# Kernel optimization log

Hardware: AMD Instinct MI355X
Metric: run time of the kernel (lower is better)

The kernel has to match this reference:

```python
import jax, jax.numpy as jnp
import numpy as np

N_NODES = 50000
N_EDGES = 800000
IN_CH = 128
HID = 32
HEADS = 4
LATENT = 64
NEG_SLOPE = 0.2  # PyG GATConv default


def setup_inputs() -> dict:
    key = jax.random.key(0)
    ks = jax.random.split(key, 12)
    HC = HID * HEADS
    inp = {
        "x": jax.random.normal(ks[0], (N_NODES, IN_CH), dtype=jnp.float32),
        "edge_index": jax.random.randint(ks[1], (2, N_EDGES), 0, N_NODES, dtype=jnp.int64),
        # GATConv params
        "W_gat": jax.random.normal(ks[2], (IN_CH, HC), dtype=jnp.float32) / np.sqrt(IN_CH),
        "b_gat": jnp.zeros((HC,), dtype=jnp.float32),
        "att_src": jax.random.normal(ks[3], (HEADS, HID), dtype=jnp.float32) / np.sqrt(HID),
        "att_dst": jax.random.normal(ks[4], (HEADS, HID), dtype=jnp.float32) / np.sqrt(HID),
        # encoder / decoder / output linears
        "W_enc": jax.random.normal(ks[5], (HC, LATENT), dtype=jnp.float32) / np.sqrt(HC),
        "b_enc": jnp.zeros((LATENT,), dtype=jnp.float32),
        "W_dec": jax.random.normal(ks[6], (LATENT, HC), dtype=jnp.float32) / np.sqrt(LATENT),
        "b_dec": jnp.zeros((HC,), dtype=jnp.float32),
        "W_out": jax.random.normal(ks[7], (HC, IN_CH), dtype=jnp.float32) / np.sqrt(HC),
        "b_out": jnp.zeros((IN_CH,), dtype=jnp.float32),
    }
    return inp


def reference(x, edge_index, W_gat, b_gat, att_src, att_dst,
              W_enc, b_enc, W_dec, b_dec, W_out, b_out):
    N = x.shape[0]
    H, C = att_src.shape
    # PyG GATConv adds self-loops by default
    loops = jnp.arange(N, dtype=edge_index.dtype)
    src = jnp.concatenate([edge_index[0], loops])  # message sources (x_j)
    dst = jnp.concatenate([edge_index[1], loops])  # aggregation targets (x_i)

    h = (x @ W_gat).reshape(N, H, C)               # [N,H,C]
    a_src = jnp.einsum('nhc,hc->nh', h, att_src)   # [N,H]
    a_dst = jnp.einsum('nhc,hc->nh', h, att_dst)   # [N,H]

    e = jax.nn.leaky_relu(a_src[src] + a_dst[dst], NEG_SLOPE)  # [E,H]
    # segment softmax over destination nodes (numerically stable)
    e_max = jax.ops.segment_max(e, dst, num_segments=N)
    e_exp = jnp.exp(e - e_max[dst])
    denom = jax.ops.segment_sum(e_exp, dst, num_segments=N)
    alpha = e_exp / (denom[dst] + 1e-16)           # [E,H]

    msg = h[src] * alpha[:, :, None]               # [E,H,C]
    agg = jax.ops.segment_sum(msg, dst, num_segments=N)  # [N,H,C]
    gat_out = agg.reshape(N, H * C) + b_gat        # concat heads + bias

    x1 = jax.nn.elu(gat_out)
    encoded = x1 @ W_enc + b_enc
    decoded = encoded @ W_dec + b_dec
    x2 = jax.nn.elu(decoded)
    return x2 @ W_out + b_out
```

## Files before the change

### kernel.cpp

```cpp
#include <hip/hip_runtime.h>
#include <hip/hip_bf16.h>

#define N_NODES 50000
#define N_EDGES 800000
#define BM 64
#define NBUCK 196
#define CAP 6144
#define CHUNK 2048
#define NB_BUCKET_BLOCKS ((N_EDGES + CHUNK - 1) / CHUNK)
#define SWZ_BLOCKS 192
#define SWZ_G 32768
#define BFT 1024

typedef _Float16 half4v __attribute__((ext_vector_type(4)));
typedef _Float16 half8 __attribute__((ext_vector_type(8)));
typedef float    float4v __attribute__((ext_vector_type(4)));

__device__ __forceinline__ float elu_f(float v) {
    return (v > 0.f) ? v : (__expf(v) - 1.f);
}

__device__ __forceinline__ unsigned f2bf2(float a, float b) {
    unsigned ua = __float_as_uint(a), ub = __float_as_uint(b);
    ua = (ua + 0x7FFFu + ((ua >> 16) & 1u)) >> 16;
    ub = (ub + 0x7FFFu + ((ub >> 16) & 1u)) >> 16;
    return ua | (ub << 16);
}
__device__ __forceinline__ float2 bf2f2(unsigned u) {
    float2 f;
    f.x = __uint_as_float(u << 16);
    f.y = __uint_as_float(u & 0xFFFF0000u);
    return f;
}

__global__ __launch_bounds__(256) void k_pre(const void* __restrict__ e_raw,
        int* __restrict__ flag,
        const float* __restrict__ We, const float* __restrict__ Wd,
        const float* __restrict__ Wo, const float* __restrict__ Wg,
        _Float16* __restrict__ swz, int* __restrict__ bcursor) {
    const int b = blockIdx.x;
    const int tid = threadIdx.x;
    if (b >= SWZ_BLOCKS) {
        __shared__ int nz;
        if (tid == 0) nz = 0;
        bcursor[tid] = 0;
        __syncthreads();
        int cnt = 0;
        const unsigned* er = (const unsigned*)e_raw;
        for (int i = tid; i < 2048; i += 256)
            if (er[2 * i + 1] != 0u) cnt = 1;
        if (cnt) atomicOr(&nz, 1);
        __syncthreads();
        if (tid == 0) *flag = (nz == 0) ? 1 : 0;
        return;
    }
    int t = b * 256 + tid;
    const float* W; int base, N;
    if (t < 8192)       { W = We; base = 0;     N = 64;  }
    else if (t < 16384) { W = Wd; base = 8192;  N = 128; }
    else if (t < 32768) { W = Wo; base = 16384; N = 128; }
    else                { W = Wg; base = SWZ_G; N = 128; }
    int loc = t - base;
    int nnt = N >> 4;
    int frag = loc >> 9, r = loc & 511, lane = r >> 3, j = r & 7;
    int kc = frag / nnt, nt = frag - kc * nnt;
    int k = kc * 32 + ((lane >> 4) << 3) + j;
    int n = nt * 16 + (lane & 15);
    swz[t] = (_Float16)W[k * N + n];
}

__global__ __launch_bounds__(256) void k_gat_lin(const float* __restrict__ x,
        const _Float16* __restrict__ swz, const float* __restrict__ att_s,
        const float* __restrict__ att_d, unsigned* __restrict__ h_bf,
        float* __restrict__ a_src, float* __restrict__ a_dst) {
    __shared__ _Float16 sx[64 * 128];
    __shared__ float sh[64 * 132];
    const int tid = threadIdx.x;
    const int m0 = blockIdx.x * 64;

#pragma unroll
    for (int i = 0; i < 8; i++) {
        int idx = tid + i * 256;
        int r = idx >> 5, c4 = idx & 31;
        int row = m0 + r; if (row >= N_NODES) row = N_NODES - 1;
        float4 v = ((const float4*)(x + (size_t)row * 128))[c4];
        half4v h;
        h[0] = (_Float16)v.x; h[1] = (_Float16)v.y;
        h[2] = (_Float16)v.z; h[3] = (_Float16)v.w;
        *(half4v*)&sx[r * 128 + c4 * 4] = h;
    }
    __syncthreads();

    const int wave = tid >> 6, lane = tid & 63;
    const int lm = lane & 15, lq = lane >> 4;
    const int wrow = wave * 16;

    {
        float4v acc[8];
#pragma unroll
        for (int nt = 0; nt < 8; nt++) acc[nt] = (float4v){0.f, 0.f, 0.f, 0.f};
#pragma unroll
        for (int kc = 0; kc < 4; kc++) {
            half8 a = *(const half8*)&sx[(wrow + lm) * 128 + kc * 32 + lq * 8];
#pragma unroll
            for (int nt = 0; nt < 8; nt++) {
                half8 b = *(const half8*)&swz[SWZ_G + (kc * 8 + nt) * 512 + lane * 8];
                acc[nt] = __builtin_amdgcn_mfma_f32_16x16x32_f16(a, b, acc[nt], 0, 0, 0);
            }
        }
#pragma unroll
        for (int nt = 0; nt < 8; nt++)
#pragma unroll
            for (int r = 0; r < 4; r++)
                sh[(wrow + lq * 4 + r) * 132 + nt * 16 + lm] = acc[nt][r];
    }
    __syncthreads();

    const int c0 = (tid & 31) * 4;
    const int r0 = (tid >> 5) * 8;
    float4 as4 = *(const float4*)&att_s[c0];
    float4 ad4 = *(const float4*)&att_d[c0];
    const int head = c0 >> 5;

#pragma unroll
    for (int r = 0; r < 8; r++) {
        int row = m0 + r0 + r;
        bool ok = row < N_NODES;
        float4 hv = *(const float4*)&sh[(r0 + r) * 132 + c0];
        if (ok) {
            uint2 p;
            p.x = f2bf2(hv.x, hv.y);
            p.y = f2bf2(hv.z, hv.w);
            *(uint2*)&h_bf[(size_t)row * 64 + (c0 >> 1)] = p;
        }
        float vs = hv.x * as4.x + hv.y * as4.y + hv.z * as4.z + hv.w * as4.w;
        float vd = hv.x * ad4.x + hv.y * ad4.y + hv.z * ad4.z + hv.w * ad4.w;
#pragma unroll
        for (int o = 4; o >= 1; o >>= 1) {
            vs += __shfl_down(vs, o, 8);
            vd += __shfl_down(vd, o, 8);
        }
        if (ok && (tid & 7) == 0) {
            a_src[row * 4 + head] = vs;
            a_dst[row * 4 + head] = vd;
        }
    }
}

__global__ __launch_bounds__(256) void k_bucket(const void* __restrict__ e_raw,
        const int* __restrict__ flag, int* __restrict__ bcursor,
        uint2* __restrict__ ebuck) {
    __shared__ int lh[256];
    __shared__ int gbase[256];
    __shared__ int lcur[256];
    const int tid = threadIdx.x;
    const int base = blockIdx.x * CHUNK;
    const int is64 = *flag;
    const long long* e64 = (const long long*)e_raw;
    const int* e32 = (const int*)e_raw;

    lh[tid] = 0;
    __syncthreads();
#pragma unroll 4
    for (int j = 0; j < CHUNK / 256; j++) {
        int e = base + j * 256 + tid;
        if (e < N_EDGES) {
            int d = is64 ? (int)e64[N_EDGES + e] : e32[N_EDGES + e];
            atomicAdd(&lh[d >> 8], 1);
        }
    }
    __syncthreads();
    if (lh[tid]) gbase[tid] = atomicAdd(&bcursor[tid], lh[tid]);
    lcur[tid] = 0;
    __syncthreads();
#pragma unroll 4
    for (int j = 0; j < CHUNK / 256; j++) {
        int e = base + j * 256 + tid;
        if (e < N_EDGES) {
            int sN, d;
            if (is64) { sN = (int)e64[e]; d = (int)e64[N_EDGES + e]; }
            else      { sN = e32[e];      d = e32[N_EDGES + e]; }
            int b = d >> 8;
            int idx = gbase[b] + atomicAdd(&lcur[b], 1);
            if (idx < CAP) {
                uint2 pr; pr.x = (unsigned)sN; pr.y = (unsigned)d;
                ebuck[b * CAP + idx] = pr;
            }
        }
    }
}

__global__ __launch_bounds__(BFT) void k_bfill(const uint2* __restrict__ ebuck,
        const int* __restrict__ bcursor, int2* __restrict__ nodeoff,
        int* __restrict__ csr_src) {
    __shared__ int lh[256];
    __shared__ int lexc[256];
    __shared__ int lcur[256];
    const int tid = threadIdx.x;
    const int b = blockIdx.x;
    const int lo = b * CAP;
    int cnt = bcursor[b]; if (cnt > CAP) cnt = CAP;
    const int hi = lo + cnt;
    const int n0 = b << 8;

    if (tid < 256) { lh[tid] = 0; lcur[tid] = 0; }
    __syncthreads();
    for (int i = lo + tid; i < hi; i += BFT)
        atomicAdd(&lh[ebuck[i].y & 255], 1);
    __syncthreads();
    {
        int v = 0;
        if (tid < 256) { v = lh[tid]; lexc[tid] = v; }
        __syncthreads();
        for (int o = 1; o < 256; o <<= 1) {
            int u = (tid < 256 && tid >= o) ? lexc[tid - o] : 0;
            __syncthreads();
            if (tid < 256) lexc[tid] += u;
            __syncthreads();
        }
        if (tid < 256) {
            int s = lexc[tid] - v;
            lexc[tid] = s;
            int node = n0 + tid;
            if (node < N_NODES) {
                int2 no; no.x = lo + s; no.y = v;
                nodeoff[node] = no;
            }
        }
    }
    __syncthreads();
    for (int i = lo + tid; i < hi; i += BFT) {
        uint2 pr = ebuck[i];
        int li = (int)(pr.y & 255);
        int p = atomicAdd(&lcur[li], 1);
        csr_src[lo + lexc[li] + p] = (int)pr.x;
    }
}

__global__ __launch_bounds__(256) void k_gather(const int2* __restrict__ nodeoff,
        const int* __restrict__ csr_src, const float* __restrict__ a_src,
        const float* __restrict__ a_dst, const unsigned* __restrict__ h_bf,
        float* __restrict__ agg) {
    int d = blockIdx.x * 4 + (threadIdx.x >> 6);
    if (d >= N_NODES) return;
    const int lane = threadIdx.x & 63;
    const int half = lane >> 5;
    const int l32 = lane & 31;
    const int hd = l32 >> 3;
    int2 nd = nodeoff[d];
    const int lo = nd.x, hi = nd.x + nd.y;

    const float adh = a_dst[d * 4 + hd];

    float den = 0.f;
    float ax = 0.f, ay = 0.f, az = 0.f, aw = 0.f;

    if (half == 0) {
        float t = a_src[d * 4 + hd] + adh;
        t = t > 0.f ? t : 0.2f * t;
        float es = __expf(t);
        den = es;
        uint2 hu = ((const uint2*)(h_bf + (size_t)d * 64))[l32];
        float2 c01 = bf2f2(hu.x), c23 = bf2f2(hu.y);
        ax = c01.x * es; ay = c01.y * es;
        az = c23.x * es; aw = c23.y * es;
    }

    int base = lo;
    for (; base + 8 <= hi; base += 8) {
        int i0 = base + half;
        int s0 = csr_src[i0 + 0];
        int s1 = csr_src[i0 + 2];
        int s2 = csr_src[i0 + 4];
        int s3 = csr_src[i0 + 6];
        uint2 u0 = ((const uint2*)(h_bf + (size_t)s0 * 64))[l32];
        uint2 u1 = ((const uint2*)(h_bf + (size_t)s1 * 64))[l32];
        uint2 u2 = ((const uint2*)(h_bf + (size_t)s2 * 64))[l32];
        uint2 u3 = ((const uint2*)(h_bf + (size_t)s3 * 64))[l32];
        float a0 = a_src[s0 * 4 + hd];
        float a1 = a_src[s1 * 4 + hd];
        float a2 = a_src[s2 * 4 + hd];
        float a3 = a_src[s3 * 4 + hd];

        float t0 = a0 + adh; t0 = t0 > 0.f ? t0 : 0.2f * t0;
        float t1 = a1 + adh; t1 = t1 > 0.f ? t1 : 0.2f * t1;
        float t2 = a2 + adh; t2 = t2 > 0.f ? t2 : 0.2f * t2;
        float t3 = a3 + adh; t3 = t3 > 0.f ? t3 : 0.2f * t3;
        float e0 = __expf(t0);
        float e1 = __expf(t1);
        float e2 = __expf(t2);
        float e3 = __expf(t3);
        den += (e0 + e1) + (e2 + e3);

        float2 p, q;
        p = bf2f2(u0.x); q = bf2f2(u0.y);
        ax = fmaf(p.x, e0, ax); ay = fmaf(p.y, e0, ay);
        az = fmaf(q.x, e0, az); aw = fmaf(q.y, e0, aw);
        p = bf2f2(u1.x); q = bf2f2(u1.y);
        ax = fmaf(p.x, e1, ax); ay = fmaf(p.y, e1, ay);
        az = fmaf(q.x, e1, az); aw = fmaf(q.y, e1, aw);
        p = bf2f2(u2.x); q = bf2f2(u2.y);
        ax = fmaf(p.x, e2, ax); ay = fmaf(p.y, e2, ay);
        az = fmaf(q.x, e2, az); aw = fmaf(q.y, e2, aw);
        p = bf2f2(u3.x); q = bf2f2(u3.y);
        ax = fmaf(p.x, e3, ax); ay = fmaf(p.y, e3, ay);
        az = fmaf(q.x, e3, az); aw = fmaf(q.y, e3, aw);
    }
    for (int i = base + half; i < hi; i += 2) {
        int s = csr_src[i];
        float tt = a_src[s * 4 + hd] + adh;
        tt = tt > 0.f ? tt : 0.2f * tt;
        float e = __expf(tt);
        den += e;
        uint2 hu = ((const uint2*)(h_bf + (size_t)s * 64))[l32];
        float2 p = bf2f2(hu.x), q = bf2f2(hu.y);
        ax = fmaf(p.x, e, ax); ay = fmaf(p.y, e, ay);
        az = fmaf(q.x, e, az); aw = fmaf(q.y, e, aw);
    }

    den += __shfl_xor(den, 32);
    ax += __shfl_xor(ax, 32);
    ay += __shfl_xor(ay, 32);
    az += __shfl_xor(az, 32);
    aw += __shfl_xor(aw, 32);

    if (half == 0) {
        float inv = 1.f / (den + 1e-16f);
        float4 o; o.x = ax * inv; o.y = ay * inv; o.z = az * inv; o.w = aw * inv;
        ((float4*)(agg + (size_t)d * 128))[l32] = o;
    }
}

__global__ __launch_bounds__(256) void k_mlp(const float* __restrict__ agg,
        const float* __restrict__ b_gat, const _Float16* __restrict__ swz,
        const float* __restrict__ b_enc, const float* __restrict__ b_dec,
        const float* __restrict__ b_out, float* __restrict__ out) {
    __shared__ _Float16 sx[64 * 128];
    __shared__ _Float16 se[4 * 16 * 64];
    const int tid = threadIdx.x;
    const int m0 = blockIdx.x * 64;

#pragma unroll
    for (int i = 0; i < 8; i++) {
        int idx = tid + i * 256;
        int r = idx >> 5, c4 = idx & 31;
        int row = m0 + r; if (row >= N_NODES) row = N_NODES - 1;
        float4 v = ((const float4*)(agg + (size_t)row * 128))[c4];
        float4 bg = ((const float4*)b_gat)[c4];
        half4v h;
        h[0] = (_Float16)elu_f(v.x + bg.x);
        h[1] = (_Float16)elu_f(v.y + bg.y);
        h[2] = (_Float16)elu_f(v.z + bg.z);
        h[3] = (_Float16)elu_f(v.w + bg.w);
        *(half4v*)&sx[r * 128 + c4 * 4] = h;
    }
    __syncthreads();

    const int wave = tid >> 6, lane = tid & 63;
    const int lm = lane & 15, lq = lane >> 4;
    const int wrow = wave * 16;
    _Float16* eslab = &se[wave * 16 * 64];

    {
        float4v acc[4];
#pragma unroll
        for (int nt = 0; nt < 4; nt++) acc[nt] = (float4v){0.f, 0.f, 0.f, 0.f};
#pragma unroll
        for (int kc = 0; kc < 4; kc++) {
            half8 a = *(const half8*)&sx[(wrow + lm) * 128 + kc * 32 + lq * 8];
#pragma unroll
            for (int nt = 0; nt < 4; nt++) {
                half8 b = *(const half8*)&swz[(kc * 4 + nt) * 512 + lane * 8];
                acc[nt] = __builtin_amdgcn_mfma_f32_16x16x32_f16(a, b, acc[nt], 0, 0, 0);
            }
        }
#pragma unroll
        for (int nt = 0; nt < 4; nt++) {
            float be = b_enc[nt * 16 + lm];
#pragma unroll
            for (int r = 0; r < 4; r++)
                eslab[(lq * 4 + r) * 64 + nt * 16 + lm] = (_Float16)(acc[nt][r] + be);
        }
    }

    {
        float4v acc[8];
#pragma unroll
        for (int nt = 0; nt < 8; nt++) acc[nt] = (float4v){0.f, 0.f, 0.f, 0.f};
#pragma unroll
        for (int kc = 0; kc < 2; kc++) {
            half8 a = *(const half8*)&eslab[lm * 64 + kc * 32 + lq * 8];
#pragma unroll
            for (int nt = 0; nt < 8; nt++) {
                half8 b = *(const half8*)&swz[8192 + (kc * 8 + nt) * 512 + lane * 8];
                acc[nt] = __builtin_amdgcn_mfma_f32_16x16x32_f16(a, b, acc[nt], 0, 0, 0);
            }
        }
#pragma unroll
        for (int nt = 0; nt < 8; nt++) {
            float bd = b_dec[nt * 16 + lm];
#pragma unroll
            for (int r = 0; r < 4; r++)
                sx[(wrow + lq * 4 + r) * 128 + nt * 16 + lm] =
                    (_Float16)elu_f(acc[nt][r] + bd);
        }
    }

    {
        float4v acc[8];
#pragma unroll
        for (int nt = 0; nt < 8; nt++) acc[nt] = (float4v){0.f, 0.f, 0.f, 0.f};
#pragma unroll
        for (int kc = 0; kc < 4; kc++) {
            half8 a = *(const half8*)&sx[(wrow + lm) * 128 + kc * 32 + lq * 8];
#pragma unroll
            for (int nt = 0; nt < 8; nt++) {
                half8 b = *(const half8*)&swz[16384 + (kc * 8 + nt) * 512 + lane * 8];
                acc[nt] = __builtin_amdgcn_mfma_f32_16x16x32_f16(a, b, acc[nt], 0, 0, 0);
            }
        }
#pragma unroll
        for (int nt = 0; nt < 8; nt++) {
            float bo = b_out[nt * 16 + lm];
#pragma unroll
            for (int r = 0; r < 4; r++) {
                int row = m0 + wrow + lq * 4 + r;
                if (row < N_NODES)
                    out[(size_t)row * 128 + nt * 16 + lm] = acc[nt][r] + bo;
            }
        }
    }
}

extern "C" void kernel_launch(void* const* d_in, const int* in_sizes, int n_in,
                              void* d_out, int out_size, void* d_ws, size_t ws_size,
                              hipStream_t stream) {
    const float* x       = (const float*)d_in[0];
    const void*  e_raw   = d_in[1];
    const float* W_gat   = (const float*)d_in[2];
    const float* b_gat   = (const float*)d_in[3];
    const float* att_src = (const float*)d_in[4];
    const float* att_dst = (const float*)d_in[5];
    const float* W_enc   = (const float*)d_in[6];
    const float* b_enc   = (const float*)d_in[7];
    const float* W_dec   = (const float*)d_in[8];
    const float* b_dec   = (const float*)d_in[9];
    const float* W_out   = (const float*)d_in[10];
    const float* b_out   = (const float*)d_in[11];
    float* out = (float*)d_out;

    float* ws      = (float*)d_ws;
    float*   hreg  = ws;
    unsigned* h_bf = (unsigned*)hreg;
    float* a_src   = hreg + 6400000;
    float* a_dst   = a_src + 200000;
    float* agg     = a_dst + 200000;
    uint2* ebuck   = (uint2*)agg;
    int*   edges   = (int*)(agg + 6400000);
    int*   csr_src = edges + 1600000;
    int2*  nodeoff = (int2*)(csr_src + NBUCK * CAP);
    int*   flag    = (int*)(nodeoff + 50000);
    int*   bcursor = flag + 1;
    _Float16* swz  = (_Float16*)(((uintptr_t)(bcursor + 256) + 15) & ~(uintptr_t)15);

    const int GBLK = (N_NODES + BM - 1) / BM;

    k_pre<<<SWZ_BLOCKS + 1, 256, 0, stream>>>(
        e_raw, flag, W_enc, W_dec, W_out, W_gat, swz, bcursor);

    k_gat_lin<<<GBLK, 256, 0, stream>>>(x, swz, att_src, att_dst, h_bf, a_src, a_dst);

    k_bucket<<<NB_BUCKET_BLOCKS, 256, 0, stream>>>(e_raw, flag, bcursor, ebuck);
    k_bfill<<<NBUCK, BFT, 0, stream>>>(ebuck, bcursor, nodeoff, csr_src);

    k_gather<<<(N_NODES + 3) / 4, 256, 0, stream>>>(nodeoff, csr_src, a_src, a_dst, h_bf, agg);

    k_mlp<<<GBLK, 256, 0, stream>>>(agg, b_gat, swz, b_enc, b_dec, b_out, out);
}
```

Before: 194.1 us.

## Fuse GAT linear with edge bucketing and pad CSR rows to multiples of eight

Merges the GAT linear-projection kernel and the edge-bucketing kernel into one launch, with disjoint block ranges doing each job. This removes a launch and lets the two independent stages overlap on the GPU. It also pads each node's CSR segment up to a multiple of 8 using -1 sentinels, so the gather loop runs only in full 8-edge steps and the scalar tail loop is gone. Padded slots cost extra masked loads that read the node's own row. CAP grows to hold the padding, and a clamp truncates a node's segment if its bucket overflows.

```diff
diff --git a/kernel.cpp b/kernel.cpp
--- a/kernel.cpp
+++ b/kernel.cpp
@@ -5,12 +5,13 @@
 #define N_EDGES 800000
 #define BM 64
 #define NBUCK 196
-#define CAP 6144
+#define CAP 8192
 #define CHUNK 2048
 #define NB_BUCKET_BLOCKS ((N_EDGES + CHUNK - 1) / CHUNK)
 #define SWZ_BLOCKS 192
 #define SWZ_G 32768
 #define BFT 1024
+#define GBLK ((N_NODES + BM - 1) / BM)
 
 typedef _Float16 half4v __attribute__((ext_vector_type(4)));
 typedef _Float16 half8 __attribute__((ext_vector_type(8)));
@@ -69,14 +70,60 @@
     swz[t] = (_Float16)W[k * N + n];
 }
 
-__global__ __launch_bounds__(256) void k_gat_lin(const float* __restrict__ x,
-        const _Float16* __restrict__ swz, const float* __restrict__ att_s,
-        const float* __restrict__ att_d, unsigned* __restrict__ h_bf,
-        float* __restrict__ a_src, float* __restrict__ a_dst) {
-    __shared__ _Float16 sx[64 * 128];
-    __shared__ float sh[64 * 132];
+__global__ __launch_bounds__(256) void k_gatlin_bucket(
+        const float* __restrict__ x, const _Float16* __restrict__ swz,
+        const float* __restrict__ att_s, const float* __restrict__ att_d,
+        unsigned* __restrict__ h_bf, float* __restrict__ a_src,
+        float* __restrict__ a_dst,
+        const void* __restrict__ e_raw, const int* __restrict__ flag,
+        int* __restrict__ bcursor, uint2* __restrict__ ebuck) {
+    __shared__ __align__(16) char smem[50176];
     const int tid = threadIdx.x;
-    const int m0 = blockIdx.x * 64;
+
+    if (blockIdx.x < NB_BUCKET_BLOCKS) {
+        int* lh    = (int*)smem;
+        int* gbase = (int*)(smem + 1024);
+        int* lcur  = (int*)(smem + 2048);
+        const int base = blockIdx.x * CHUNK;
+        const int is64 = *flag;
+        const long long* e64 = (const long long*)e_raw;
+        const int* e32 = (const int*)e_raw;
+
+        lh[tid] = 0;
+        __syncthreads();
+#pragma unroll 4
+        for (int j = 0; j < CHUNK / 256; j++) {
+            int e = base + j * 256 + tid;
+            if (e < N_EDGES) {
+                int d = is64 ? (int)e64[N_EDGES + e] : e32[N_EDGES + e];
+                atomicAdd(&lh[d >> 8], 1);
+            }
+        }
+        __syncthreads();
+        if (lh[tid]) gbase[tid] = atomicAdd(&bcursor[tid], lh[tid]);
+        lcur[tid] = 0;
+        __syncthreads();
+#pragma unroll 4
+        for (int j = 0; j < CHUNK / 256; j++) {
+            int e = base + j * 256 + tid;
+            if (e < N_EDGES) {
+                int sN, d;
+                if (is64) { sN = (int)e64[e]; d = (int)e64[N_EDGES + e]; }
+                else      { sN = e32[e];      d = e32[N_EDGES + e]; }
+                int bb = d >> 8;
+                int idx = gbase[bb] + atomicAdd(&lcur[bb], 1);
+                if (idx < CAP) {
+                    uint2 pr; pr.x = (unsigned)sN; pr.y = (unsigned)d;
+                    ebuck[bb * CAP + idx] = pr;
+                }
+            }
+        }
+        return;
+    }
+
+    _Float16* sx = (_Float16*)smem;
+    float*    sh = (float*)(smem + 16384);
+    const int m0 = (blockIdx.x - NB_BUCKET_BLOCKS) * 64;
 
 #pragma unroll
     for (int i = 0; i < 8; i++) {
@@ -143,49 +190,6 @@
         if (ok && (tid & 7) == 0) {
             a_src[row * 4 + head] = vs;
             a_dst[row * 4 + head] = vd;
-        }
-    }
-}
-
-__global__ __launch_bounds__(256) void k_bucket(const void* __restrict__ e_raw,
-        const int* __restrict__ flag, int* __restrict__ bcursor,
-        uint2* __restrict__ ebuck) {
-    __shared__ int lh[256];
-    __shared__ int gbase[256];
-    __shared__ int lcur[256];
-    const int tid = threadIdx.x;
-    const int base = blockIdx.x * CHUNK;
-    const int is64 = *flag;
-    const long long* e64 = (const long long*)e_raw;
-    const int* e32 = (const int*)e_raw;
-
-    lh[tid] = 0;
-    __syncthreads();
-#pragma unroll 4
-    for (int j = 0; j < CHUNK / 256; j++) {
-        int e = base + j * 256 + tid;
-        if (e < N_EDGES) {
-            int d = is64 ? (int)e64[N_EDGES + e] : e32[N_EDGES + e];
-            atomicAdd(&lh[d >> 8], 1);
-        }
-    }
-    __syncthreads();
-    if (lh[tid]) gbase[tid] = atomicAdd(&bcursor[tid], lh[tid]);
-    lcur[tid] = 0;
-    __syncthreads();
-#pragma unroll 4
-    for (int j = 0; j < CHUNK / 256; j++) {
-        int e = base + j * 256 + tid;
-        if (e < N_EDGES) {
-            int sN, d;
-            if (is64) { sN = (int)e64[e]; d = (int)e64[N_EDGES + e]; }
-            else      { sN = e32[e];      d = e32[N_EDGES + e]; }
-            int b = d >> 8;
-            int idx = gbase[b] + atomicAdd(&lcur[b], 1);
-            if (idx < CAP) {
-                uint2 pr; pr.x = (unsigned)sN; pr.y = (unsigned)d;
-                ebuck[b * CAP + idx] = pr;
-            }
         }
     }
 }
@@ -208,32 +212,44 @@
     for (int i = lo + tid; i < hi; i += BFT)
         atomicAdd(&lh[ebuck[i].y & 255], 1);
     __syncthreads();
-    {
-        int v = 0;
-        if (tid < 256) { v = lh[tid]; lexc[tid] = v; }
-        __syncthreads();
-        for (int o = 1; o < 256; o <<= 1) {
-            int u = (tid < 256 && tid >= o) ? lexc[tid - o] : 0;
-            __syncthreads();
-            if (tid < 256) lexc[tid] += u;
-            __syncthreads();
-        }
-        if (tid < 256) {
-            int s = lexc[tid] - v;
-            lexc[tid] = s;
-            int node = n0 + tid;
-            if (node < N_NODES) {
-                int2 no; no.x = lo + s; no.y = v;
-                nodeoff[node] = no;
-            }
-        }
-    }
-    __syncthreads();
+
+    int v = 0, p = 0;
+    if (tid < 256) {
+        v = lh[tid];
+        p = (v + 7) & ~7;
+        lexc[tid] = p;
+    }
+    __syncthreads();
+    for (int o = 1; o < 256; o <<= 1) {
+        int u = (tid < 256 && tid >= o) ? lexc[tid - o] : 0;
+        __syncthreads();
+        if (tid < 256) lexc[tid] += u;
+        __syncthreads();
+    }
+    if (tid < 256) {
+        int s = lexc[tid] - p;
+        lexc[tid] = s;
+        int node = n0 + tid;
+        if (node < N_NODES) {
+            int2 no;
+            no.x = lo + s;
+            int maxlen = CAP - s; if (maxlen < 0) maxlen = 0;
+            no.y = p <= maxlen ? p : (maxlen & ~7);
+            nodeoff[node] = no;
+        }
+    }
+    __syncthreads();
+
     for (int i = lo + tid; i < hi; i += BFT) {
         uint2 pr = ebuck[i];
         int li = (int)(pr.y & 255);
-        int p = atomicAdd(&lcur[li], 1);
-        csr_src[lo + lexc[li] + p] = (int)pr.x;
+        int pos = atomicAdd(&lcur[li], 1);
+        int dst = lexc[li] + pos;
+        if (dst < CAP) csr_src[lo + dst] = (int)pr.x;
+    }
+    if (tid < 256) {
+        int base = lexc[tid];
+        for (int j = v; j < p && base + j < CAP; j++) csr_src[lo + base + j] = -1;
     }
 }
 
@@ -266,30 +282,33 @@
         az = c23.x * es; aw = c23.y * es;
     }
 
-    int base = lo;
-    for (; base + 8 <= hi; base += 8) {
+    for (int base = lo; base < hi; base += 8) {
         int i0 = base + half;
         int s0 = csr_src[i0 + 0];
         int s1 = csr_src[i0 + 2];
         int s2 = csr_src[i0 + 4];
         int s3 = csr_src[i0 + 6];
-        uint2 u0 = ((const uint2*)(h_bf + (size_t)s0 * 64))[l32];
-        uint2 u1 = ((const uint2*)(h_bf + (size_t)s1 * 64))[l32];
-        uint2 u2 = ((const uint2*)(h_bf + (size_t)s2 * 64))[l32];
-        uint2 u3 = ((const uint2*)(h_bf + (size_t)s3 * 64))[l32];
-        float a0 = a_src[s0 * 4 + hd];
-        float a1 = a_src[s1 * 4 + hd];
-        float a2 = a_src[s2 * 4 + hd];
-        float a3 = a_src[s3 * 4 + hd];
+        int g0 = s0 < 0 ? d : s0;
+        int g1 = s1 < 0 ? d : s1;
+        int g2 = s2 < 0 ? d : s2;
+        int g3 = s3 < 0 ? d : s3;
+        uint2 u0 = ((const uint2*)(h_bf + (size_t)g0 * 64))[l32];
+        uint2 u1 = ((const uint2*)(h_bf + (size_t)g1 * 64))[l32];
+        uint2 u2 = ((const uint2*)(h_bf + (size_t)g2 * 64))[l32];
+        uint2 u3 = ((const uint2*)(h_bf + (size_t)g3 * 64))[l32];
+        float a0 = a_src[g0 * 4 + hd];
+        float a1 = a_src[g1 * 4 + hd];
+        float a2 = a_src[g2 * 4 + hd];
+        float a3 = a_src[g3 * 4 + hd];
 
         float t0 = a0 + adh; t0 = t0 > 0.f ? t0 : 0.2f * t0;
         float t1 = a1 + adh; t1 = t1 > 0.f ? t1 : 0.2f * t1;
         float t2 = a2 + adh; t2 = t2 > 0.f ? t2 : 0.2f * t2;
         float t3 = a3 + adh; t3 = t3 > 0.f ? t3 : 0.2f * t3;
-        float e0 = __expf(t0);
-        float e1 = __expf(t1);
-        float e2 = __expf(t2);
-        float e3 = __expf(t3);
+        float e0 = s0 < 0 ? 0.f : __expf(t0);
+        float e1 = s1 < 0 ? 0.f : __expf(t1);
+        float e2 = s2 < 0 ? 0.f : __expf(t2);
+        float e3 = s3 < 0 ? 0.f : __expf(t3);
         den += (e0 + e1) + (e2 + e3);
 
         float2 p, q;
@@ -305,17 +324,6 @@
         p = bf2f2(u3.x); q = bf2f2(u3.y);
         ax = fmaf(p.x, e3, ax); ay = fmaf(p.y, e3, ay);
         az = fmaf(q.x, e3, az); aw = fmaf(q.y, e3, aw);
-    }
-    for (int i = base + half; i < hi; i += 2) {
-        int s = csr_src[i];
-        float tt = a_src[s * 4 + hd] + adh;
-        tt = tt > 0.f ? tt : 0.2f * tt;
-        float e = __expf(tt);
-        den += e;
-        uint2 hu = ((const uint2*)(h_bf + (size_t)s * 64))[l32];
-        float2 p = bf2f2(hu.x), q = bf2f2(hu.y);
-        ax = fmaf(p.x, e, ax); ay = fmaf(p.y, e, ay);
-        az = fmaf(q.x, e, az); aw = fmaf(q.y, e, aw);
     }
 
     den += __shfl_xor(den, 32);
@@ -456,21 +464,19 @@
     float* a_dst   = a_src + 200000;
     float* agg     = a_dst + 200000;
     uint2* ebuck   = (uint2*)agg;
-    int*   edges   = (int*)(agg + 6400000);
-    int*   csr_src = edges + 1600000;
+    int*   csr_src = (int*)(agg + 6400000);
     int2*  nodeoff = (int2*)(csr_src + NBUCK * CAP);
     int*   flag    = (int*)(nodeoff + 50000);
     int*   bcursor = flag + 1;
     _Float16* swz  = (_Float16*)(((uintptr_t)(bcursor + 256) + 15) & ~(uintptr_t)15);
 
-    const int GBLK = (N_NODES + BM - 1) / BM;
-
     k_pre<<<SWZ_BLOCKS + 1, 256, 0, stream>>>(
         e_raw, flag, W_enc, W_dec, W_out, W_gat, swz, bcursor);
 
-    k_gat_lin<<<GBLK, 256, 0, stream>>>(x, swz, att_src, att_dst, h_bf, a_src, a_dst);
-
-    k_bucket<<<NB_BUCKET_BLOCKS, 256, 0, stream>>>(e_raw, flag, bcursor, ebuck);
+    k_gatlin_bucket<<<NB_BUCKET_BLOCKS + GBLK, 256, 0, stream>>>(
+        x, swz, att_src, att_dst, h_bf, a_src, a_dst,
+        e_raw, flag, bcursor, ebuck);
+
     k_bfill<<<NBUCK, BFT, 0, stream>>>(ebuck, bcursor, nodeoff, csr_src);
 
     k_gather<<<(N_NODES + 3) / 4, 256, 0, stream>>>(nodeoff, csr_src, a_src, a_dst, h_bf, agg);
```

Result: faster. 187.4 us (-3.5%).
